# Kernel optimization log

Measured on AMD Instinct MI355X. Metric: run time of the kernel, lower is better.

## Reference

```python
import jax, jax.numpy as jnp
import numpy as np

DIM = 256
HEADS = 8
WS = 8      # window size
SS = 4      # shift size
EPS = 1e-5
HEAD_DIM = DIM // HEADS
SCALE = HEAD_DIM ** (-0.5)
N = WS * WS

# relative position index, replicating tf.meshgrid default 'xy' indexing
_ch = np.arange(WS)
_coords = np.stack(np.meshgrid(_ch, _ch, indexing='xy'))          # [2, WS, WS]
_flat = _coords.reshape(2, -1)                                     # [2, N]
_rel = _flat[:, :, None] - _flat[:, None, :]                       # [2, N, N]
_rel = _rel.transpose(1, 2, 0) + np.array([WS - 1, WS - 1])
_rel = _rel * np.array([2 * WS - 1, 1])
RPI = jnp.asarray(_rel.sum(-1).reshape(-1))                        # [N*N] int


def _calc_mask(H, W):
    # faithful to source: mask is -100 where window region ids are EQUAL, 0 otherwise
    img = np.zeros((H, W))
    slices = (slice(0, -WS), slice(-WS, -SS), slice(-SS, None))
    cnt = 0
    for hs in slices:
        for ws_ in slices:
            img[hs, ws_] = cnt
            cnt += 1
    mw = img.reshape(H // WS, WS, W // WS, WS).transpose(0, 2, 1, 3).reshape(-1, N)
    diff = mw[:, None, :] - mw[:, :, None]
    mask = np.where(diff == 0, -100.0, 0.0).astype(np.float32)     # [nW, N, N]
    return jnp.asarray(mask)


def _layernorm(x, g, b):
    m = jnp.mean(x, axis=-1, keepdims=True)
    v = jnp.mean(jnp.square(x - m), axis=-1, keepdims=True)
    return (x - m) * jax.lax.rsqrt(v + EPS) * g + b


def setup_inputs() -> dict:
    key = jax.random.key(0)
    ks = jax.random.split(key, 8)
    B, L, C = 16, 64 * 64, DIM
    s = 0.02
    return {
        'x': jax.random.normal(ks[0], (B, L, C), jnp.float32),
        'norm1_g': jnp.ones((C,), jnp.float32),
        'norm1_b': jnp.zeros((C,), jnp.float32),
        'qkv_w': jax.random.normal(ks[1], (C, 3 * C), jnp.float32) * s,
        'qkv_b': jnp.zeros((3 * C,), jnp.float32),
        'rpb_table': jax.random.normal(ks[2], ((2 * WS - 1) ** 2, HEADS), jnp.float32) * s,
        'proj_w': jax.random.normal(ks[3], (C, C), jnp.float32) * s,
        'proj_b': jnp.zeros((C,), jnp.float32),
        'norm2_g': jnp.ones((C,), jnp.float32),
        'norm2_b': jnp.zeros((C,), jnp.float32),
        'fc1_w': jax.random.normal(ks[4], (C, 4 * C), jnp.float32) * s,
        'fc1_b': jnp.zeros((4 * C,), jnp.float32),
        'fc2_w': jax.random.normal(ks[5], (4 * C, C), jnp.float32) * s,
        'fc2_b': jnp.zeros((C,), jnp.float32),
        'h': 64,
        'w': 64,
    }


def reference(x, norm1_g, norm1_b, qkv_w, qkv_b, rpb_table, proj_w, proj_b,
              norm2_g, norm2_b, fc1_w, fc1_b, fc2_w, fc2_b, h, w):
    B, L, C = x.shape
    nH, nW = h // WS, w // WS
    nWin = nH * nW
    shortcut = x

    xn = _layernorm(x, norm1_g, norm1_b).reshape(B, h, w, C)
    xn = jnp.roll(xn, shift=(-SS, -SS), axis=(1, 2))                 # cyclic shift
    # window partition -> [B*nWin, N, C]
    xw = xn.reshape(B, nH, WS, nW, WS, C).transpose(0, 1, 3, 2, 4, 5).reshape(B * nWin, N, C)

    qkv = (xw @ qkv_w + qkv_b).reshape(B * nWin, N, 3, HEADS, HEAD_DIM)
    qkv = qkv.transpose(2, 0, 3, 1, 4)                               # [3, B*nWin, H, N, d]
    q, k, v = qkv[0] * SCALE, qkv[1], qkv[2]

    attn = jnp.einsum('bhnd,bhmd->bhnm', q, k)                       # [B*nWin, H, N, N]
    bias = rpb_table[RPI].reshape(N, N, HEADS).transpose(2, 0, 1)    # [H, N, N]
    attn = attn + bias[None]

    mask = _calc_mask(h, w)                                          # [nWin, N, N]
    attn = attn.reshape(B, nWin, HEADS, N, N) + mask[None, :, None]
    attn = jax.nn.softmax(attn, axis=-1).reshape(B * nWin, HEADS, N, N)

    out = jnp.einsum('bhnm,bhmd->bhnd', attn, v)                     # [B*nWin, H, N, d]
    out = out.transpose(0, 2, 1, 3).reshape(B * nWin, N, C)
    out = out @ proj_w + proj_b

    # window reverse + reverse shift
    out = out.reshape(B, nH, nW, WS, WS, C).transpose(0, 1, 3, 2, 4, 5).reshape(B, h, w, C)
    out = jnp.roll(out, shift=(SS, SS), axis=(1, 2)).reshape(B, h * w, C)

    y = shortcut + out
    m = _layernorm(y, norm2_g, norm2_b)
    m = jax.nn.gelu(m @ fc1_w + fc1_b, approximate=False) @ fc2_w + fc2_b
    # faithful to source: final residual reuses the ORIGINAL shortcut, not y
    return shortcut + m
```

## Files before the change

### kernel.cpp

```cpp
#include <hip/hip_runtime.h>
#include <math.h>

typedef __bf16 bf16;
typedef __bf16 bf16x4 __attribute__((ext_vector_type(4)));
typedef __bf16 bf16x8 __attribute__((ext_vector_type(8)));
typedef float f32x4 __attribute__((ext_vector_type(4)));

#define AS1 __attribute__((address_space(1)))
#define AS3 __attribute__((address_space(3)))

__device__ __forceinline__ void gload_lds16(const bf16* g, bf16* l) {
    __builtin_amdgcn_global_load_lds((const AS1 void*)g, (AS3 void*)l, 16, 0, 0);
}

__device__ __forceinline__ float gelu_fast(float v) {
    const float u = 1.5957691216057308f * (v + 0.044715f * v * v * v);
    return v / (1.0f + __expf(-u));
}

__global__ __launch_bounds__(256)
void wprep_all(const float* __restrict__ qkv_w, const float* __restrict__ proj_w,
               const float* __restrict__ fc1_w, const float* __restrict__ fc2_w,
               bf16* __restrict__ qkv_wt, bf16* __restrict__ proj_wt,
               bf16* __restrict__ fc1_wt, bf16* __restrict__ fc2_wt)
{
    int idx = blockIdx.x * 256 + threadIdx.x;
    const float* src; bf16* dst; int K, N;
    if (idx < 196608)            { src = qkv_w;  dst = qkv_wt;  K = 256;  N = 768; }
    else if (idx < 262144)       { idx -= 196608; src = proj_w; dst = proj_wt; K = 256;  N = 256; }
    else if (idx < 524288)       { idx -= 262144; src = fc1_w;  dst = fc1_wt;  K = 256;  N = 1024; }
    else                         { idx -= 524288; src = fc2_w;  dst = fc2_wt;  K = 1024; N = 256; }
    const int k = idx / N, n = idx % N;
    dst[(long)n * K + k] = (bf16)src[idx];
}

__global__ __launch_bounds__(256)
void ln1_window(const float* __restrict__ x, const float* __restrict__ g,
                const float* __restrict__ be, bf16* __restrict__ xw)
{
    const int t = threadIdx.x;
    const int lane = t & 63;
    const int w = t >> 6;
    const long tok = (long)blockIdx.x * 4 + w;
    const float4 v = ((const float4*)(x + tok * 256))[lane];
    float sum = v.x + v.y + v.z + v.w;
    float sq  = v.x * v.x + v.y * v.y + v.z * v.z + v.w * v.w;
#pragma unroll
    for (int m = 32; m >= 1; m >>= 1) {
        sum += __shfl_xor(sum, m, 64);
        sq  += __shfl_xor(sq,  m, 64);
    }
    const float mean = sum * (1.0f / 256.0f);
    const float var  = sq * (1.0f / 256.0f) - mean * mean;
    const float rstd = rsqrtf(var + 1e-5f);
    const float4 gv = ((const float4*)g)[lane];
    const float4 bv = ((const float4*)be)[lane];
    bf16x4 ov;
    ov[0] = (bf16)((v.x - mean) * rstd * gv.x + bv.x);
    ov[1] = (bf16)((v.y - mean) * rstd * gv.y + bv.y);
    ov[2] = (bf16)((v.z - mean) * rstd * gv.z + bv.z);
    ov[3] = (bf16)((v.w - mean) * rstd * gv.w + bv.w);
    const int b = (int)(tok >> 12);
    const int l = (int)(tok & 4095);
    const int i = l >> 6, j = l & 63;
    const int ip = (i + 60) & 63, jp = (j + 60) & 63;
    const int winl = ((ip >> 3) << 3) + (jp >> 3);
    const int n = ((ip & 7) << 3) + (jp & 7);
    const long drow = ((long)b * 64 + winl) * 64 + n;
    *(bf16x4*)(xw + drow * 256 + lane * 4) = ov;
}

__global__ __launch_bounds__(256)
void ln2_kernel(const float* __restrict__ x, const bf16* __restrict__ pj,
                const float* __restrict__ g, const float* __restrict__ be,
                bf16* __restrict__ xn2)
{
    const int t = threadIdx.x;
    const int lane = t & 63;
    const int w = t >> 6;
    const long tok = (long)blockIdx.x * 4 + w;
    const float4 xv = ((const float4*)(x + tok * 256))[lane];
    const bf16x4 pv = *(const bf16x4*)(pj + tok * 256 + lane * 4);
    float y0 = xv.x + (float)pv[0];
    float y1 = xv.y + (float)pv[1];
    float y2 = xv.z + (float)pv[2];
    float y3 = xv.w + (float)pv[3];
    float sum = y0 + y1 + y2 + y3;
    float sq  = y0 * y0 + y1 * y1 + y2 * y2 + y3 * y3;
#pragma unroll
    for (int m = 32; m >= 1; m >>= 1) {
        sum += __shfl_xor(sum, m, 64);
        sq  += __shfl_xor(sq,  m, 64);
    }
    const float mean = sum * (1.0f / 256.0f);
    const float var  = sq * (1.0f / 256.0f) - mean * mean;
    const float rstd = rsqrtf(var + 1e-5f);
    const float4 gv = ((const float4*)g)[lane];
    const float4 bv = ((const float4*)be)[lane];
    bf16x4 ov;
    ov[0] = (bf16)((y0 - mean) * rstd * gv.x + bv.x);
    ov[1] = (bf16)((y1 - mean) * rstd * gv.y + bv.y);
    ov[2] = (bf16)((y2 - mean) * rstd * gv.z + bv.z);
    ov[3] = (bf16)((y3 - mean) * rstd * gv.w + bv.w);
    *(bf16x4*)(xn2 + tok * 256 + lane * 4) = ov;
}

template<int EPI, int KT>
__global__ __launch_bounds__(512, 2)
void gemm_w(const bf16* __restrict__ A, const bf16* __restrict__ Bt,
            const float* __restrict__ bias, void* __restrict__ outp,
            int N, const float* __restrict__ xres, void* __restrict__ aux,
            int gx, int nb)
{
    constexpr int K = KT * 32;
    extern __shared__ bf16 lds[];
    bf16* sA = lds;
    bf16* sB = lds + 3 * 8192;
    const int t = threadIdx.x;
    const int l = t & 63;
    const int w = t >> 6;
    const int wr = w >> 1, wc = w & 1;
    const int q = nb >> 3;
    const int id = ((int)blockIdx.x & 7) * q + ((int)blockIdx.x >> 3);
    const long m0 = (long)(id / gx) * 256;
    const long n0 = (long)(id % gx) * 128;

    const bf16* asrcp[2]; bf16* adstp[2];
#pragma unroll
    for (int j = 0; j < 2; j++) {
        const int idx = j * 512 + t;
        const int p = idx >> 3, s = idx & 7;
        const int sl = s ^ (p & 7);
        const int row = 2 * p + (sl >> 2);
        const int ce = (sl & 3) * 8;
        asrcp[j] = A + (m0 + row) * (long)K + ce;
        adstp[j] = &sA[idx * 8];
    }
    const bf16* bsrcp; bf16* bdstp;
    {
        const int p = t >> 3, s = t & 7;
        const int sl = s ^ (p & 7);
        const int row = 2 * p + (sl >> 2);
        const int ce = (sl & 3) * 8;
        bsrcp = Bt + (n0 + row) * (long)K + ce;
        bdstp = &sB[t * 8];
    }

    const int c = l >> 4;
    int eA[4], eB[4];
#pragma unroll
    for (int i = 0; i < 4; i++) {
        const int rowA = wr * 64 + (l & 15) + i * 16;
        const int pa = rowA >> 1;
        eA[i] = (pa * 8 + ((((rowA & 1) << 2) + c) ^ (pa & 7))) * 8;
        const int rowB = wc * 64 + (l & 15) + i * 16;
        const int pb = rowB >> 1;
        eB[i] = (pb * 8 + ((((rowB & 1) << 2) + c) ^ (pb & 7))) * 8;
    }

    f32x4 acc[4][4];
#pragma unroll
    for (int i = 0; i < 4; i++)
#pragma unroll
        for (int j = 0; j < 4; j++) acc[i][j] = (f32x4){0.f, 0.f, 0.f, 0.f};

#define STAGE(bufi, ko)                                                        \
    do {                                                                       \
        gload_lds16(asrcp[0] + (ko), adstp[0] + (bufi) * 8192);                \
        gload_lds16(asrcp[1] + (ko), adstp[1] + (bufi) * 8192);                \
        gload_lds16(bsrcp + (ko), bdstp + (bufi) * 4096);                      \
    } while (0)

    STAGE(0, 0);
    STAGE(1, 32);

#pragma unroll
    for (int kt = 0; kt < KT; ++kt) {
        const int buf = kt % 3;
        if (kt < KT - 1)
            asm volatile("s_waitcnt vmcnt(3)" ::: "memory");
        else
            asm volatile("s_waitcnt vmcnt(0)" ::: "memory");
        __builtin_amdgcn_s_barrier();
        __builtin_amdgcn_sched_barrier(0);
        if (kt + 2 < KT)
            STAGE((kt + 2) % 3, (kt + 2) * 32);
        bf16x8 av[4], bv[4];
#pragma unroll
        for (int ni = 0; ni < 4; ni++)
            bv[ni] = *(const bf16x8*)&sB[buf * 4096 + eB[ni]];
#pragma unroll
        for (int mi = 0; mi < 4; mi++)
            av[mi] = *(const bf16x8*)&sA[buf * 8192 + eA[mi]];
#pragma unroll
        for (int mi = 0; mi < 4; mi++)
#pragma unroll
            for (int ni = 0; ni < 4; ni++)
                acc[mi][ni] = __builtin_amdgcn_mfma_f32_16x16x32_bf16(
                    bv[ni], av[mi], acc[mi][ni], 0, 0, 0);
    }
#undef STAGE

#pragma unroll
    for (int mi = 0; mi < 4; mi++)
#pragma unroll
        for (int ni = 0; ni < 4; ni++) {
            const long row = m0 + wr * 64 + mi * 16 + (l & 15);
            const int col = (int)(n0 + wc * 64 + ni * 16 + (l >> 4) * 4);
            const float4 bz = *(const float4*)&bias[col];
            float vv[4];
            vv[0] = acc[mi][ni][0] + bz.x;
            vv[1] = acc[mi][ni][1] + bz.y;
            vv[2] = acc[mi][ni][2] + bz.z;
            vv[3] = acc[mi][ni][3] + bz.w;
            if constexpr (EPI == 2) {
#pragma unroll
                for (int j = 0; j < 4; j++) vv[j] = gelu_fast(vv[j]);
            }
            if constexpr (EPI == 3) {
                const float4 xr = *(const float4*)&xres[row * N + col];
                float4 ov = {vv[0] + xr.x, vv[1] + xr.y, vv[2] + xr.z, vv[3] + xr.w};
                *(float4*)&((float*)outp)[row * N + col] = ov;
            } else if constexpr (EPI == 0) {
                if (col >= 512) {
                    bf16* vt = (bf16*)aux;
                    const int win = (int)(row >> 6);
                    const int n = (int)(row & 63);
#pragma unroll
                    for (int j = 0; j < 4; j++)
                        vt[(long)win * 16384 + (col - 512 + j) * 64 + n] = (bf16)vv[j];
                } else {
                    bf16x4 ov;
#pragma unroll
                    for (int j = 0; j < 4; j++) ov[j] = (bf16)vv[j];
                    *(bf16x4*)&((bf16*)outp)[row * N + col] = ov;
                }
            } else {
                bf16x4 ov;
#pragma unroll
                for (int j = 0; j < 4; j++) ov[j] = (bf16)vv[j];
                if constexpr (EPI == 1) {
                    const int gwin = (int)(row >> 6);
                    const int n = (int)(row & 63);
                    const int bb = gwin >> 6, wi = gwin & 63;
                    const int ipp = ((wi >> 3) << 3) + (n >> 3);
                    const int jpp = ((wi & 7) << 3) + (n & 7);
                    const int ii = (ipp + 4) & 63, jj = (jpp + 4) & 63;
                    const long tok = ((long)bb << 12) + (ii << 6) + jj;
                    *(bf16x4*)&((bf16*)outp)[tok * 256 + col] = ov;
                } else {
                    *(bf16x4*)&((bf16*)outp)[row * N + col] = ov;
                }
            }
        }
    (void)xres; (void)aux;
}

__global__ __launch_bounds__(256, 4)
void attn_kernel(const bf16* __restrict__ qkv, const bf16* __restrict__ vT,
                 const float* __restrict__ rpb, bf16* __restrict__ out)
{
    __shared__ bf16 P_lds[4][64 * 64];
    const int t = threadIdx.x;
    const int lane = t & 63;
    const int w = t >> 6;
    const int win = blockIdx.x >> 1;
    const int head = (blockIdx.x & 1) * 4 + w;
    const int wi = win & 63;
    const int lr = lane & 15;
    const int lg = lane >> 4;
    const int lk = lg * 8;
    const long base = (long)win * 64 * 768;
    const float scale = 0.17677669529663687f;
    const int whb = (wi >> 3) << 3;
    const int wwb = (wi & 7) << 3;
    const f32x4 z4 = {0.f, 0.f, 0.f, 0.f};

    const bf16* qp  = qkv + base + head * 32;
    const bf16* kp  = qkv + base + 256 + head * 32;
    const bf16* vtp = vT + (long)win * 16384 + head * 32 * 64;

    int idm[4];
#pragma unroll
    for (int ni = 0; ni < 4; ni++) {
        const int m = ni * 16 + lr;
        const int gi2 = whb + (m >> 3), gj2 = wwb + (m & 7);
        idm[ni] = (gi2 < 56 ? 0 : (gi2 < 60 ? 1 : 2)) * 3 + (gj2 < 56 ? 0 : (gj2 < 60 ? 1 : 2));
    }

    bf16x8 aq[4], bk[4];
#pragma unroll
    for (int mi = 0; mi < 4; mi++)
        aq[mi] = *(const bf16x8*)(qp + (mi * 16 + lr) * 768 + lk);
#pragma unroll
    for (int ni = 0; ni < 4; ni++)
        bk[ni] = *(const bf16x8*)(kp + (ni * 16 + lr) * 768 + lk);

    f32x4 s[4][4];
#pragma unroll
    for (int i = 0; i < 4; i++)
#pragma unroll
        for (int j = 0; j < 4; j++) s[i][j] = z4;
#pragma unroll
    for (int mi = 0; mi < 4; mi++)
#pragma unroll
        for (int ni = 0; ni < 4; ni++)
            s[mi][ni] = __builtin_amdgcn_mfma_f32_16x16x32_bf16(aq[mi], bk[ni], s[mi][ni], 0, 0, 0);

#pragma unroll
    for (int mi = 0; mi < 4; mi++)
#pragma unroll
        for (int r = 0; r < 4; r++) {
            const int n = mi * 16 + lg * 4 + r;
            const int gi = whb + (n >> 3);
            const int gj = wwb + (n & 7);
            const int idn = (gi < 56 ? 0 : (gi < 60 ? 1 : 2)) * 3 + (gj < 56 ? 0 : (gj < 60 ? 1 : 2));
            float vals[4];
            float rowmax = -3.0e38f;
#pragma unroll
            for (int ni = 0; ni < 4; ni++) {
                const int m = ni * 16 + lr;
                const int dj = (n & 7) - (m & 7);
                const int di = (n >> 3) - (m >> 3);
                float sv = s[mi][ni][r] * scale + rpb[((dj + 7) * 15 + (di + 7)) * 8 + head];
                if (idn == idm[ni]) sv -= 100.0f;
                vals[ni] = sv;
                rowmax = fmaxf(rowmax, sv);
            }
#pragma unroll
            for (int msk = 8; msk >= 1; msk >>= 1)
                rowmax = fmaxf(rowmax, __shfl_xor(rowmax, msk, 64));
            float rsum = 0.f;
#pragma unroll
            for (int ni = 0; ni < 4; ni++) {
                const float p = __expf(vals[ni] - rowmax);
                vals[ni] = p;
                rsum += p;
            }
#pragma unroll
            for (int msk = 8; msk >= 1; msk >>= 1)
                rsum += __shfl_xor(rsum, msk, 64);
            const float inv = 1.0f / rsum;
            const int swz = (n & 7) << 3;
#pragma unroll
            for (int ni = 0; ni < 4; ni++)
                P_lds[w][n * 64 + ((ni * 16 + lr) ^ swz)] = (bf16)(vals[ni] * inv);
        }

    f32x4 o[4][2];
#pragma unroll
    for (int i = 0; i < 4; i++)
#pragma unroll
        for (int j = 0; j < 2; j++) o[i][j] = z4;
#pragma unroll
    for (int kk = 0; kk < 2; kk++) {
        bf16x8 bv[2];
#pragma unroll
        for (int ni = 0; ni < 2; ni++)
            bv[ni] = *(const bf16x8*)&vtp[(ni * 16 + lr) * 64 + kk * 32 + lk];
#pragma unroll
        for (int mi = 0; mi < 4; mi++) {
            const int row = mi * 16 + lr;
            const bf16x8 ap = *(const bf16x8*)&P_lds[w][row * 64 + ((kk * 32 + lk) ^ ((row & 7) << 3))];
#pragma unroll
            for (int ni = 0; ni < 2; ni++)
                o[mi][ni] = __builtin_amdgcn_mfma_f32_16x16x32_bf16(bv[ni], ap, o[mi][ni], 0, 0, 0);
        }
    }
#pragma unroll
    for (int mi = 0; mi < 4; mi++)
#pragma unroll
        for (int ni = 0; ni < 2; ni++) {
            const int n = mi * 16 + lr;
            const int d = ni * 16 + lg * 4;
            bf16x4 ov;
            ov[0] = (bf16)o[mi][ni][0]; ov[1] = (bf16)o[mi][ni][1];
            ov[2] = (bf16)o[mi][ni][2]; ov[3] = (bf16)o[mi][ni][3];
            *(bf16x4*)(out + ((long)(win * 64 + n)) * 256 + head * 32 + d) = ov;
        }
}

extern "C" void kernel_launch(void* const* d_in, const int* in_sizes, int n_in,
                              void* d_out, int out_size, void* d_ws, size_t ws_size,
                              hipStream_t stream)
{
    (void)in_sizes; (void)n_in; (void)out_size;
    const float* x      = (const float*)d_in[0];
    const float* n1g    = (const float*)d_in[1];
    const float* n1b    = (const float*)d_in[2];
    const float* qkv_w  = (const float*)d_in[3];
    const float* qkv_b  = (const float*)d_in[4];
    const float* rpb    = (const float*)d_in[5];
    const float* proj_w = (const float*)d_in[6];
    const float* proj_b = (const float*)d_in[7];
    const float* n2g    = (const float*)d_in[8];
    const float* n2b    = (const float*)d_in[9];
    const float* fc1_w  = (const float*)d_in[10];
    const float* fc1_b  = (const float*)d_in[11];
    const float* fc2_w  = (const float*)d_in[12];
    const float* fc2_b  = (const float*)d_in[13];
    float* out = (float*)d_out;

    char* ws = (char*)d_ws;
    bf16* qkv_wt  = (bf16*)(ws + 0);
    bf16* proj_wt = (bf16*)(ws + 393216);
    bf16* fc1_wt  = (bf16*)(ws + 524288);
    bf16* fc2_wt  = (bf16*)(ws + 1048576);
    bf16* xw      = (bf16*)(ws + 2097152);
    bf16* qkvb    = (bf16*)(ws + 35651584);
    bf16* attn_o  = xw;
    bf16* proj_o  = qkvb;
    bf16* vT      = (bf16*)d_out;
    bf16* xn2     = (bf16*)d_out;
    bf16* hbuf    = xw;
    if (ws_size < 136314880ull) return;

    const size_t LB = 73728;

    wprep_all<<<3072, 256, 0, stream>>>(qkv_w, proj_w, fc1_w, fc2_w,
                                        qkv_wt, proj_wt, fc1_wt, fc2_wt);

    ln1_window<<<16384, 256, 0, stream>>>(x, n1g, n1b, xw);
    gemm_w<0, 8><<<1536, 512, LB, stream>>>(xw, qkv_wt, qkv_b, qkvb, 768, nullptr, vT, 6, 1536);
    attn_kernel<<<2048, 256, 0, stream>>>(qkvb, vT, rpb, attn_o);
    gemm_w<1, 8><<<512, 512, LB, stream>>>(attn_o, proj_wt, proj_b, proj_o, 256, nullptr, nullptr, 2, 512);
    ln2_kernel<<<16384, 256, 0, stream>>>(x, proj_o, n2g, n2b, xn2);
    gemm_w<2, 8><<<2048, 512, LB, stream>>>(xn2, fc1_wt, fc1_b, hbuf, 1024, nullptr, nullptr, 8, 2048);
    gemm_w<3, 32><<<512, 512, LB, stream>>>(hbuf, fc2_wt, fc2_b, out, 256, x, nullptr, 2, 512);
}
```

Measured before the change: 281.8 us.

## Add 256x256-tile GEMM kernel with triple-buffered LDS for QKV and FC1

Adds a new GEMM variant that computes 256x256 output tiles per 512-thread block, with a 3-stage async global-to-LDS pipeline and swizzled LDS layout. It is used for the QKV and FC1 projections, halving the block count and raising operand reuse per LDS load. The cost is larger LDS use (96KB) and more accumulator registers per thread, which limits occupancy to about 2 blocks per CU and may cause spills or a tail effect with fewer blocks.

```diff
diff --git a/kernel.cpp b/kernel.cpp
--- a/kernel.cpp
+++ b/kernel.cpp
@@ -256,6 +256,140 @@
     (void)xres; (void)aux;
 }
 
+template<int EPI, int KT>
+__global__ __launch_bounds__(512, 2)
+void gemm_big(const bf16* __restrict__ A, const bf16* __restrict__ Bt,
+              const float* __restrict__ bias, void* __restrict__ outp,
+              int N, const float* __restrict__ xres, void* __restrict__ aux,
+              int gx, int nb)
+{
+    constexpr int K = KT * 32;
+    extern __shared__ bf16 lds[];
+    bf16* sA = lds;
+    bf16* sB = lds + 3 * 8192;
+    const int t = threadIdx.x;
+    const int l = t & 63;
+    const int w = t >> 6;
+    const int wr = w >> 1, wc = w & 1;
+    const int q = nb >> 3;
+    const int id = ((int)blockIdx.x & 7) * q + ((int)blockIdx.x >> 3);
+    const long m0 = (long)(id / gx) * 256;
+    const long n0 = (long)(id % gx) * 256;
+
+    const bf16* asrcp[2]; bf16* adstp[2];
+    const bf16* bsrcp[2]; bf16* bdstp[2];
+#pragma unroll
+    for (int j = 0; j < 2; j++) {
+        const int idx = j * 512 + t;
+        const int p = idx >> 3, s = idx & 7;
+        const int sl = s ^ (p & 7);
+        const int row = 2 * p + (sl >> 2);
+        const int ce = (sl & 3) * 8;
+        asrcp[j] = A + (m0 + row) * (long)K + ce;
+        adstp[j] = &sA[idx * 8];
+        bsrcp[j] = Bt + (n0 + row) * (long)K + ce;
+        bdstp[j] = &sB[idx * 8];
+    }
+
+    const int c = l >> 4;
+    int eA[4], eB[8];
+#pragma unroll
+    for (int i = 0; i < 4; i++) {
+        const int rowA = wr * 64 + (l & 15) + i * 16;
+        const int pa = rowA >> 1;
+        eA[i] = (pa * 8 + ((((rowA & 1) << 2) + c) ^ (pa & 7))) * 8;
+    }
+#pragma unroll
+    for (int i = 0; i < 8; i++) {
+        const int rowB = wc * 128 + (l & 15) + i * 16;
+        const int pb = rowB >> 1;
+        eB[i] = (pb * 8 + ((((rowB & 1) << 2) + c) ^ (pb & 7))) * 8;
+    }
+
+    f32x4 acc[4][8];
+#pragma unroll
+    for (int i = 0; i < 4; i++)
+#pragma unroll
+        for (int j = 0; j < 8; j++) acc[i][j] = (f32x4){0.f, 0.f, 0.f, 0.f};
+
+#define STAGE(bufi, ko)                                                        \
+    do {                                                                       \
+        gload_lds16(asrcp[0] + (ko), adstp[0] + (bufi) * 8192);                \
+        gload_lds16(asrcp[1] + (ko), adstp[1] + (bufi) * 8192);                \
+        gload_lds16(bsrcp[0] + (ko), bdstp[0] + (bufi) * 8192);                \
+        gload_lds16(bsrcp[1] + (ko), bdstp[1] + (bufi) * 8192);                \
+    } while (0)
+
+    STAGE(0, 0);
+    STAGE(1, 32);
+
+#pragma unroll
+    for (int kt = 0; kt < KT; ++kt) {
+        const int buf = kt % 3;
+        if (kt < KT - 1)
+            asm volatile("s_waitcnt vmcnt(4)" ::: "memory");
+        else
+            asm volatile("s_waitcnt vmcnt(0)" ::: "memory");
+        __builtin_amdgcn_s_barrier();
+        __builtin_amdgcn_sched_barrier(0);
+        if (kt + 2 < KT)
+            STAGE((kt + 2) % 3, (kt + 2) * 32);
+        bf16x8 av[4], bv[8];
+#pragma unroll
+        for (int ni = 0; ni < 8; ni++)
+            bv[ni] = *(const bf16x8*)&sB[buf * 8192 + eB[ni]];
+#pragma unroll
+        for (int mi = 0; mi < 4; mi++)
+            av[mi] = *(const bf16x8*)&sA[buf * 8192 + eA[mi]];
+#pragma unroll
+        for (int mi = 0; mi < 4; mi++)
+#pragma unroll
+            for (int ni = 0; ni < 8; ni++)
+                acc[mi][ni] = __builtin_amdgcn_mfma_f32_16x16x32_bf16(
+                    bv[ni], av[mi], acc[mi][ni], 0, 0, 0);
+    }
+#undef STAGE
+
+#pragma unroll
+    for (int mi = 0; mi < 4; mi++)
+#pragma unroll
+        for (int ni = 0; ni < 8; ni++) {
+            const long row = m0 + wr * 64 + mi * 16 + (l & 15);
+            const int col = (int)(n0 + wc * 128 + ni * 16 + (l >> 4) * 4);
+            const float4 bz = *(const float4*)&bias[col];
+            float vv[4];
+            vv[0] = acc[mi][ni][0] + bz.x;
+            vv[1] = acc[mi][ni][1] + bz.y;
+            vv[2] = acc[mi][ni][2] + bz.z;
+            vv[3] = acc[mi][ni][3] + bz.w;
+            if constexpr (EPI == 2) {
+#pragma unroll
+                for (int j = 0; j < 4; j++) vv[j] = gelu_fast(vv[j]);
+            }
+            if constexpr (EPI == 0) {
+                if (col >= 512) {
+                    bf16* vt = (bf16*)aux;
+                    const int win = (int)(row >> 6);
+                    const int n = (int)(row & 63);
+#pragma unroll
+                    for (int j = 0; j < 4; j++)
+                        vt[(long)win * 16384 + (col - 512 + j) * 64 + n] = (bf16)vv[j];
+                } else {
+                    bf16x4 ov;
+#pragma unroll
+                    for (int j = 0; j < 4; j++) ov[j] = (bf16)vv[j];
+                    *(bf16x4*)&((bf16*)outp)[row * N + col] = ov;
+                }
+            } else {
+                bf16x4 ov;
+#pragma unroll
+                for (int j = 0; j < 4; j++) ov[j] = (bf16)vv[j];
+                *(bf16x4*)&((bf16*)outp)[row * N + col] = ov;
+            }
+        }
+    (void)xres; (void)aux;
+}
+
 __global__ __launch_bounds__(256, 4)
 void attn_kernel(const bf16* __restrict__ qkv, const bf16* __restrict__ vT,
                  const float* __restrict__ rpb, bf16* __restrict__ out)
@@ -415,16 +549,17 @@
     bf16* hbuf    = xw;
     if (ws_size < 136314880ull) return;
 
-    const size_t LB = 73728;
+    const size_t LB  = 73728;
+    const size_t LB2 = 98304;
 
     wprep_all<<<3072, 256, 0, stream>>>(qkv_w, proj_w, fc1_w, fc2_w,
                                         qkv_wt, proj_wt, fc1_wt, fc2_wt);
 
     ln1_window<<<16384, 256, 0, stream>>>(x, n1g, n1b, xw);
-    gemm_w<0, 8><<<1536, 512, LB, stream>>>(xw, qkv_wt, qkv_b, qkvb, 768, nullptr, vT, 6, 1536);
+    gemm_big<0, 8><<<768, 512, LB2, stream>>>(xw, qkv_wt, qkv_b, qkvb, 768, nullptr, vT, 3, 768);
     attn_kernel<<<2048, 256, 0, stream>>>(qkvb, vT, rpb, attn_o);
     gemm_w<1, 8><<<512, 512, LB, stream>>>(attn_o, proj_wt, proj_b, proj_o, 256, nullptr, nullptr, 2, 512);
     ln2_kernel<<<16384, 256, 0, stream>>>(x, proj_o, n2g, n2b, xn2);
-    gemm_w<2, 8><<<2048, 512, LB, stream>>>(xn2, fc1_wt, fc1_b, hbuf, 1024, nullptr, nullptr, 8, 2048);
+    gemm_big<2, 8><<<1024, 512, LB2, stream>>>(xn2, fc1_wt, fc1_b, hbuf, 1024, nullptr, nullptr, 4, 1024);
     gemm_w<3, 32><<<512, 512, LB, stream>>>(hbuf, fc2_wt, fc2_b, out, 256, x, nullptr, 2, 512);
 }
```

Result: slower. 298.2 us (+5.8%).
